# Kernel tuning notes

Measured on AMD Instinct MI355X. Metric: run time of the kernel, lower is better.

## Reference

```python
import jax, jax.numpy as jnp
import numpy as np

B, N, D = 1, 4096, 512
H, HD = 8, 64
NBINS = 512
CAND = 64
SCALE = 1.0 / np.sqrt(HD)
MAX_NORM = 1.0 - 1e-5
TWO_PI = 2.0 * np.pi


def _project(x):
    # Poincare-ball style projection: clip L2 norm of each point to MAX_NORM.
    n = jnp.sqrt(jnp.sum(x * x, axis=-1, keepdims=True))
    s = jnp.minimum(1.0, MAX_NORM / jnp.maximum(n, 1e-12))
    return x * s


def _bins(x):
    # Deterministic geometric binning (DavisCache stand-in): quantize the
    # angle of the first two coordinates into NBINS bins.
    ang = jnp.arctan2(x[..., 1], x[..., 0])  # (-pi, pi]
    b = jnp.floor((ang / TWO_PI + 0.5) * NBINS)
    return jnp.clip(b, 0, NBINS - 1).astype(jnp.int32)


def setup_inputs() -> dict:
    key0 = jax.random.key(0)
    ks = jax.random.split(key0, 12)
    w = 0.02  # typical init scale for projection weights
    return {
        "query": jax.random.normal(ks[0], (B, N, D), dtype=jnp.float32),
        "key": jax.random.normal(ks[1], (B, N, D), dtype=jnp.float32),
        "value": jax.random.normal(ks[2], (B, N, D), dtype=jnp.float32),
        "Wq": jax.random.normal(ks[3], (D, D), dtype=jnp.float32) * w,
        "bq": jnp.zeros((D,), dtype=jnp.float32),
        "Wk": jax.random.normal(ks[4], (D, D), dtype=jnp.float32) * w,
        "bk": jnp.zeros((D,), dtype=jnp.float32),
        "Wv": jax.random.normal(ks[5], (D, D), dtype=jnp.float32) * w,
        "bv": jnp.zeros((D,), dtype=jnp.float32),
        "Wo": jax.random.normal(ks[6], (D, D), dtype=jnp.float32) * w,
        "bo": jnp.zeros((D,), dtype=jnp.float32),
    }


def reference(query, key, value, Wq, bq, Wk, bk, Wv, bv, Wo, bo):
    Bq, Nq, Dm = query.shape
    Nk = key.shape[1]
    # projections + split heads -> (B, H, N, HD)
    q = (query @ Wq.T + bq).reshape(Bq, Nq, H, HD).transpose(0, 2, 1, 3)
    k = (key @ Wk.T + bk).reshape(Bq, Nk, H, HD).transpose(0, 2, 1, 3)
    v = (value @ Wv.T + bv).reshape(Bq, Nk, H, HD).transpose(0, 2, 1, 3)
    q = _project(q)
    k = _project(k)

    # geometric binning; candidate keys for a query are those whose bin is
    # within radius 1 of the query's bin (neighboring_bins, radius=1).
    qb = _bins(q)  # (B, H, Nq) int32
    kb = _bins(k)  # (B, H, Nk) int32
    mask = jnp.abs(qb[..., :, None] - kb[..., None, :]) <= 1  # (B,H,Nq,Nk)
    # fallback: if a query has no candidates, attend over all keys
    any_valid = jnp.any(mask, axis=-1, keepdims=True)
    eff = jnp.where(any_valid, mask, True)
    # keep only the first CAND candidates per query (by key index)
    rank = jnp.cumsum(eff.astype(jnp.int32), axis=-1) - 1
    sel = eff & (rank < CAND)

    scores = jnp.einsum("bhqd,bhkd->bhqk", q, k) * SCALE
    scores = jnp.where(sel, scores, -jnp.inf)
    attn = jax.nn.softmax(scores, axis=-1)  # dropout p=0.0 (eval mode)
    out = jnp.einsum("bhqk,bhkd->bhqd", attn, v)

    out = out.transpose(0, 2, 1, 3).reshape(Bq, Nq, Dm)
    return out @ Wo.T + bo
```

## Files before the change

### kernel.cpp

```cpp
#include <hip/hip_runtime.h>
#include <math.h>

typedef unsigned short u16;
typedef __attribute__((ext_vector_type(8))) short v8bf;
typedef __attribute__((ext_vector_type(4))) float f32x4;

#define N_TOK 4096
#define DMODEL 512
#define NHEAD 8
#define HDIM 64
#define CANDN 64
#define NBINS 512
#define BINCAP 64
#define QCAP 128
#define ATT_SCALE 0.125f
#define MAX_NORM_F 0.99999f

__device__ __forceinline__ float bf2f(u16 u) {
  union { unsigned int i; float f; } v; v.i = ((unsigned int)u) << 16; return v.f;
}
__device__ __forceinline__ u16 f2bf(float f) {
  union { float f; unsigned int i; } v; v.f = f;
  unsigned int x = v.i;
  return (u16)((x + 0x7fffu + ((x >> 16) & 1u)) >> 16);
}
__device__ __forceinline__ uint4 load_pack8(const float* __restrict__ p) {
  const float4 x0 = *(const float4*)p;
  const float4 x1 = *(const float4*)(p + 4);
  union { u16 h[8]; uint4 u; } r;
  r.h[0] = f2bf(x0.x); r.h[1] = f2bf(x0.y); r.h[2] = f2bf(x0.z); r.h[3] = f2bf(x0.w);
  r.h[4] = f2bf(x1.x); r.h[5] = f2bf(x1.y); r.h[6] = f2bf(x1.z); r.h[7] = f2bf(x1.w);
  return r.u;
}

__device__ __forceinline__ void gload16(const u16* __restrict__ g, u16* l) {
  __builtin_amdgcn_global_load_lds(
      (const __attribute__((address_space(1))) void*)g,
      (__attribute__((address_space(3))) void*)l, 16, 0, 0);
}

__global__ __launch_bounds__(256) void prep_kernel(
    const float* __restrict__ query, const float* __restrict__ key_,
    const float* __restrict__ value,
    const float* __restrict__ Wq, const float* __restrict__ Wk,
    const float* __restrict__ Wv, const float* __restrict__ Wo,
    u16* __restrict__ qx, u16* __restrict__ kx, u16* __restrict__ vx,
    u16* __restrict__ wqx, u16* __restrict__ wkx, u16* __restrict__ wvx,
    u16* __restrict__ wox,
    int* __restrict__ qb, int* __restrict__ kb, unsigned char* __restrict__ flags,
    int* __restrict__ khist)
{
  __shared__ float xs[16 * 516];
  const int blk = blockIdx.x;
  const int tid = threadIdx.x;

  if (blk >= 4096) {
    int4 z4; z4.x = 0; z4.y = 0; z4.z = 0; z4.w = 0;
    ((int4*)khist)[((blk - 4096) << 8) + tid] = z4;
    return;
  }

  if (blk >= 512) {
    const int rel = blk - 512;
    const float* src; u16* dst; int base;
    if (rel < 1024)      { src = query; dst = qx; base = rel << 11; }
    else if (rel < 2048) { src = key_;  dst = kx; base = (rel - 1024) << 11; }
    else if (rel < 3072) { src = value; dst = vx; base = (rel - 2048) << 11; }
    else {
      const int r2 = rel - 3072; const int w = r2 >> 7;
      src = (w == 0) ? Wq : (w == 1) ? Wk : (w == 2) ? Wv : Wo;
      dst = (w == 0) ? wqx : (w == 1) ? wkx : (w == 2) ? wvx : wox;
      base = (r2 & 127) << 11;
    }
    const int off = base + tid * 8;
    *(uint4*)(dst + off) = load_pack8(src + off);
    return;
  }

  const int isk  = blk >> 8;
  const int tile = blk & 255;
  const float* X = isk ? key_ : query;
  const float* W = isk ? Wk : Wq;

#pragma unroll
  for (int i = 0; i < 8; ++i) {
    const int flat = i * 1024 + tid * 4;
    const int row = flat >> 9, col = flat & 511;
    *(float4*)&xs[row * 516 + col] = *(const float4*)(X + (tile * 16 + row) * DMODEL + col);
  }
  __syncthreads();

  const int n_local = tid >> 4;
  const int pair = tid & 15;
  const int h = pair >> 1, coord = pair & 1;
  const float* wrow = W + ((h << 6) + coord) * DMODEL;
  const float* xrow = &xs[n_local * 516];

  double c0 = 0.0, c1 = 0.0, c2 = 0.0, c3 = 0.0;
  for (int k = 0; k < DMODEL; k += 4) {
    const float4 xv = *(const float4*)(xrow + k);
    const float4 wv = *(const float4*)(wrow + k);
    c0 = fma((double)xv.x, (double)wv.x, c0);
    c1 = fma((double)xv.y, (double)wv.y, c1);
    c2 = fma((double)xv.z, (double)wv.z, c2);
    c3 = fma((double)xv.w, (double)wv.w, c3);
  }
  const double a = (c0 + c1) + (c2 + c3);
  const double other = __shfl_xor(a, 1);
  if (coord == 0) {
    const double a0 = a, a1 = other;
    const int n = tile * 16 + n_local;
    double ang = atan2(a1, a0);
    double t = (ang / 6.283185307179586 + 0.5) * 512.0;
    int b = (int)floor(t);
    b = b < 0 ? 0 : (b > 511 ? 511 : b);
    (isk ? kb : qb)[(h << 12) + n] = b;

    const double r = sqrt(a0 * a0 + a1 * a1);
    const double dist = fabs(t - nearbyint(t));
    const double margin = fmin(0.45, 3.3e-4 / fmax(r, 1e-30) + 5e-5);
    flags[(isk << 15) | (h << 12) | n] = (dist < margin) ? 1 : 0;
  }
}

__device__ float fdlibm_atanf(float x) {
#pragma clang fp contract(off)
  const float atanhi[4] = {4.6364760399e-01f, 7.8539812565e-01f,
                           9.8279368877e-01f, 1.5707962513e+00f};
  const float atanlo[4] = {5.0121582440e-09f, 3.7748947079e-08f,
                           3.4473217170e-08f, 7.5497894159e-08f};
  const float aT[5] = {3.3333328366e-01f, -1.9999158382e-01f, 1.4253635705e-01f,
                       -1.0648017377e-01f, 6.1687607318e-02f};
  unsigned ix = __float_as_uint(x);
  const unsigned sign = ix >> 31;
  ix &= 0x7fffffffu;
  int id;
  float z, w, s1, s2;
  if (ix >= 0x4c800000u) {
    z = atanhi[3] + 0x1p-120f;
    return sign ? -z : z;
  }
  if (ix < 0x3ee00000u) {
    if (ix < 0x39800000u) return x;
    id = -1;
  } else {
    x = fabsf(x);
    if (ix < 0x3f980000u) {
      if (ix < 0x3f300000u) { id = 0; x = (2.0f * x - 1.0f) / (2.0f + x); }
      else                  { id = 1; x = (x - 1.0f) / (x + 1.0f); }
    } else {
      if (ix < 0x401c0000u) { id = 2; x = (x - 1.5f) / (1.0f + 1.5f * x); }
      else                  { id = 3; x = -1.0f / x; }
    }
  }
  z = x * x;
  w = z * z;
  s1 = z * (aT[0] + w * (aT[2] + w * aT[4]));
  s2 = w * (aT[1] + w * aT[3]);
  if (id < 0) return x - x * (s1 + s2);
  z = atanhi[id] - ((x * (s1 + s2) - atanlo[id]) - x);
  return sign ? -z : z;
}

__device__ float fdlibm_atan2f(float y, float x) {
#pragma clang fp contract(off)
  const float pi = 3.1415927410e+00f, pi_lo = -8.7422776573e-08f;
  const unsigned hx = __float_as_uint(x), hy = __float_as_uint(y);
  if (hx == 0x3f800000u) return fdlibm_atanf(y);
  const unsigned m = ((hy >> 31) & 1u) | ((hx >> 30) & 2u);
  const unsigned ix = hx & 0x7fffffffu, iy = hy & 0x7fffffffu;
  if (iy == 0u) {
    switch (m) { case 0: case 1: return y; case 2: return pi; default: return -pi; }
  }
  if (ix == 0u) return (m & 1u) ? -1.57079637050628662f : 1.57079637050628662f;
  float z;
  if (ix + (26u << 23) < iy) {
    z = 1.57079637050628662f;
    return (m & 1u) ? -z : z;
  }
  if ((m & 2u) && iy + (26u << 23) < ix) z = 0.0f;
  else z = fdlibm_atanf(fabsf(y / x));
  switch (m) {
    case 0: return z;
    case 1: return -z;
    case 2: return pi - (z - pi_lo);
    default: return (z - pi_lo) - pi;
  }
}

__global__ __launch_bounds__(256) void gemmfix_kernel(
    const u16* __restrict__ qx, const u16* __restrict__ kx, const u16* __restrict__ vx,
    const u16* __restrict__ wqx, const u16* __restrict__ wkx, const u16* __restrict__ wvx,
    const float* __restrict__ bq, const float* __restrict__ bk, const float* __restrict__ bv,
    const float* __restrict__ query, const float* __restrict__ key_,
    const float* __restrict__ Wq, const float* __restrict__ Wk,
    const unsigned char* __restrict__ flags,
    int* __restrict__ qb, int* __restrict__ kb,
    u16* __restrict__ Qb, u16* __restrict__ Kb, u16* __restrict__ Vb)
{
  __shared__ u16 As[128 * 32];
  __shared__ u16 Ws[128 * 32];
  __shared__ int wle[64];
  __shared__ int wlc;

  const int blk = blockIdx.x;
  const int tid = threadIdx.x;

  if (blk >= 384) {
    const int slice = blk - 384;
    if (tid == 0) wlc = 0;
    __syncthreads();
    for (int i = tid; i < 1024; i += 256) {
      const int flat = slice * 1024 + i;
      if (flags[flat]) {
        const int p = atomicAdd(&wlc, 1);
        if (p < 64) wle[p] = flat;
      }
    }
    __syncthreads();
    int nw = wlc; if (nw > 64) nw = 64;
    const int w = tid >> 6, d = tid & 63;
    for (int e = w; e < nw; e += 4) {
      const int flat = wle[e];
      const int n = flat & 4095;
      const int h = (flat >> 12) & 7;
      const int isk = flat >> 15;
      const float* xr = (isk ? key_ : query) + n * DMODEL;
      const float* wr = (isk ? Wk : Wq) + ((h << 6) + d) * DMODEL;
      float acc = 0.0f;
      for (int k = 0; k < DMODEL; k += 16) {
        const float4 xa = *(const float4*)(xr + k);
        const float4 xb = *(const float4*)(xr + k + 4);
        const float4 xc = *(const float4*)(xr + k + 8);
        const float4 xd = *(const float4*)(xr + k + 12);
        const float4 wa = *(const float4*)(wr + k);
        const float4 wb = *(const float4*)(wr + k + 4);
        const float4 wc = *(const float4*)(wr + k + 8);
        const float4 wd = *(const float4*)(wr + k + 12);
        acc = __fmaf_rn(xa.x, wa.x, acc); acc = __fmaf_rn(xa.y, wa.y, acc);
        acc = __fmaf_rn(xa.z, wa.z, acc); acc = __fmaf_rn(xa.w, wa.w, acc);
        acc = __fmaf_rn(xb.x, wb.x, acc); acc = __fmaf_rn(xb.y, wb.y, acc);
        acc = __fmaf_rn(xb.z, wb.z, acc); acc = __fmaf_rn(xb.w, wb.w, acc);
        acc = __fmaf_rn(xc.x, wc.x, acc); acc = __fmaf_rn(xc.y, wc.y, acc);
        acc = __fmaf_rn(xc.z, wc.z, acc); acc = __fmaf_rn(xc.w, wc.w, acc);
        acc = __fmaf_rn(xd.x, wd.x, acc); acc = __fmaf_rn(xd.y, wd.y, acc);
        acc = __fmaf_rn(xd.z, wd.z, acc); acc = __fmaf_rn(xd.w, wd.w, acc);
      }
      {
#pragma clang fp contract(off)
        const float sq = acc * acc;
        float rr[8];
#pragma unroll
        for (int j = 0; j < 8; ++j) rr[j] = __shfl(sq, j);
        for (int i = 8; i < 64; i += 8) {
#pragma unroll
          for (int j = 0; j < 8; ++j) rr[j] += __shfl(sq, i + j);
        }
        const float ss = ((rr[0] + rr[1]) + (rr[2] + rr[3])) +
                         ((rr[4] + rr[5]) + (rr[6] + rr[7]));
        const float nrm = __fsqrt_rn(ss);
        const float s = fminf(1.0f, 0.99999f / fmaxf(nrm, 1e-12f));
        const float c0 = __shfl(acc, 0) * s;
        const float c1 = __shfl(acc, 1) * s;
        const float cr = (float)atan2((double)c1, (double)c0);
        const float fd = fdlibm_atan2f(c1, c0);
        const float tol = fmaxf(fabsf(cr) * 6e-7f, 1e-30f);
        const float ang = (fabsf(fd - cr) <= tol) ? fd : cr;
        const float t = ((ang / 6.2831854820251465f) + 0.5f) * 512.0f;
        int b = (int)floorf(t);
        b = b < 0 ? 0 : (b > 511 ? 511 : b);
        if (d == 0) (isk ? kb : qb)[(h << 12) + n] = b;
      }
    }
    return;
  }

  const int z = blk >> 7;
  const int rem = blk & 127;
  const int bm = (rem & 31) * 128;
  const int bn = (rem >> 5) * 128;

  const u16* A    = (z == 0) ? qx : (z == 1) ? kx : vx;
  const u16* W    = (z == 0) ? wqx : (z == 1) ? wkx : wvx;
  const float* bias = (z == 0) ? bq : (z == 1) ? bk : bv;
  u16* O          = (z == 0) ? Qb : (z == 1) ? Kb : Vb;

  const int lane = tid & 63;
  const int wave = tid >> 6;
  const int wm = (wave & 1) * 64;
  const int wn = (wave >> 1) * 64;
  const int l15 = lane & 15;
  const int quad = lane >> 4;

  const int ca = tid;
  const int cb = tid + 256;
  const int ra = ca >> 2, oa = (ca & 3) * 8;
  const int rb = cb >> 2, ob = (cb & 3) * 8;

  f32x4 acc[4][4] = {};

  for (int kt = 0; kt < DMODEL; kt += 32) {
    __syncthreads();
    gload16(A + (bm + ra) * DMODEL + kt + oa, &As[ca * 8]);
    gload16(A + (bm + rb) * DMODEL + kt + ob, &As[cb * 8]);
    gload16(W + (bn + ra) * DMODEL + kt + oa, &Ws[ca * 8]);
    gload16(W + (bn + rb) * DMODEL + kt + ob, &Ws[cb * 8]);
    __syncthreads();
    v8bf af[4], bfr[4];
#pragma unroll
    for (int i = 0; i < 4; ++i)
      af[i] = *(const v8bf*)&As[(wm + i * 16 + l15) * 32 + quad * 8];
#pragma unroll
    for (int j = 0; j < 4; ++j)
      bfr[j] = *(const v8bf*)&Ws[(wn + j * 16 + l15) * 32 + quad * 8];
#pragma unroll
    for (int i = 0; i < 4; ++i)
#pragma unroll
      for (int j = 0; j < 4; ++j)
        acc[i][j] = __builtin_amdgcn_mfma_f32_16x16x32_bf16(af[i], bfr[j], acc[i][j], 0, 0, 0);
  }

  float bval[4];
#pragma unroll
  for (int j = 0; j < 4; ++j) bval[j] = bias[bn + wn + j * 16 + l15];
  const int h = (bn + wn) >> 6;

#pragma unroll
  for (int i = 0; i < 4; ++i) {
#pragma unroll
    for (int r = 0; r < 4; ++r) {
      const int row = bm + wm + i * 16 + quad * 4 + r;
      float v0 = acc[i][0][r] + bval[0];
      float v1 = acc[i][1][r] + bval[1];
      float v2 = acc[i][2][r] + bval[2];
      float v3 = acc[i][3][r] + bval[3];
      if (z != 2) {
        float ss = v0 * v0 + v1 * v1 + v2 * v2 + v3 * v3;
#pragma unroll
        for (int o = 1; o < 16; o <<= 1) ss += __shfl_xor(ss, o);
        const float s = fminf(1.0f, MAX_NORM_F / fmaxf(sqrtf(ss), 1e-12f));
        v0 *= s; v1 *= s; v2 *= s; v3 *= s;
      }
      const int base = (((h << 12) + row) << 6) + l15;
      O[base +  0] = f2bf(v0); O[base + 16] = f2bf(v1);
      O[base + 32] = f2bf(v2); O[base + 48] = f2bf(v3);
    }
  }
}

__global__ __launch_bounds__(256) void bin_hist_kernel(
    const int* __restrict__ kb, const int* __restrict__ qb,
    int* __restrict__ khist, u16* __restrict__ blist,
    int* __restrict__ qhist, u16* __restrict__ qlist)
{
  const int h = blockIdx.x;
  const int type = blockIdx.y;
  const int* src = type ? qb : kb;
  int* hist = type ? qhist : khist;
  u16* list = type ? qlist : blist;
  const int cap = type ? QCAP : BINCAP;

  const int i = blockIdx.z * 256 + threadIdx.x;
  const int b = src[(h << 12) + i];
  const int pos = atomicAdd(&hist[(h << 9) + b], 1);
  if (pos < cap) list[((h << 9) + b) * cap + pos] = (u16)i;
}

__global__ __launch_bounds__(64) void attn_bin_kernel(
    const u16* __restrict__ Qb, const u16* __restrict__ Kb,
    const u16* __restrict__ Vb, const int* __restrict__ qhist,
    const u16* __restrict__ qlist, const int* __restrict__ khist,
    const u16* __restrict__ blist, u16* __restrict__ aout)
{
  __shared__ u16 kf[4 * 2 * 4 * 16 * 8];
  __shared__ u16 vf[4 * 2 * 4 * 16 * 8];
  __shared__ u16 pf[16 * 72];
  __shared__ u16 s_cand[64];
  __shared__ int s_qg[16];

  const int hb = blockIdx.x;
  const int h = hb >> 9;
  const int b = hb & 511;
  int qcnt = qhist[hb];
  if (qcnt > QCAP) qcnt = QCAP;
  if (qcnt == 0) return;

  const int lane = threadIdx.x;
  const int l15 = lane & 15;
  const int quad = lane >> 4;

  int v0 = 0xFFFF, v1 = 0xFFFF, v2 = 0xFFFF;
  int c0 = 0, c1 = 0, c2 = 0;
  if (b > 0) {
    c0 = khist[(h << 9) + b - 1];
    if (c0 > BINCAP) c0 = BINCAP;
    if (lane < c0) v0 = (int)blist[(((h << 9) + b - 1) << 6) + lane];
  }
  {
    c1 = khist[(h << 9) + b];
    if (c1 > BINCAP) c1 = BINCAP;
    if (lane < c1) v1 = (int)blist[(((h << 9) + b) << 6) + lane];
  }
  if (b < NBINS - 1) {
    c2 = khist[(h << 9) + b + 1];
    if (c2 > BINCAP) c2 = BINCAP;
    if (lane < c2) v2 = (int)blist[(((h << 9) + b + 1) << 6) + lane];
  }

  int r0 = 0, r1 = 0, r2 = 0;
#pragma unroll 8
  for (int j = 0; j < 64; ++j) {
    const int w0 = __shfl(v0, j);
    const int w1 = __shfl(v1, j);
    const int w2 = __shfl(v2, j);
    r0 += (w0 < v0) + (w1 < v0) + (w2 < v0);
    r1 += (w0 < v1) + (w1 < v1) + (w2 < v1);
    r2 += (w0 < v2) + (w1 < v2) + (w2 < v2);
  }
  const int tot = c0 + c1 + c2;
  const int ccnt = tot < CANDN ? tot : CANDN;
  const int ccnt_eff = (tot == 0) ? 64 : ccnt;
  if (tot == 0) {
    s_cand[lane] = (u16)lane;
  } else {
    if (v0 != 0xFFFF && r0 < CANDN) s_cand[r0] = (u16)v0;
    if (v1 != 0xFFFF && r1 < CANDN) s_cand[r1] = (u16)v1;
    if (v2 != 0xFFFF && r2 < CANDN) s_cand[r2] = (u16)v2;
  }
  __syncthreads();
  if (tot > 0 && lane >= ccnt) s_cand[lane] = s_cand[0];
  __syncthreads();

  {
    const int r = lane >> 3, s = lane & 7;
    const int ks = s >> 2, qd = s & 3;
#pragma unroll
    for (int it = 0; it < 8; ++it) {
      const int key = it * 8 + r;
      const int c = s_cand[key];
      const uint4 kv = *(const uint4*)(Kb + ((h << 18) | (c << 6)) + s * 8);
      const int idx = ((((key >> 4) * 2 + ks) * 4 + qd) * 16 + (key & 15)) * 8;
      *(uint4*)&kf[idx] = kv;
    }
  }
  {
    const int r = lane >> 3, s = lane & 7;
    const int nt = s >> 1, d0 = (s & 1) * 8;
#pragma unroll
    for (int it = 0; it < 8; ++it) {
      const int key = it * 8 + r;
      const int c = s_cand[key];
      union { u16 hh[8]; uint4 u; } vv;
      vv.u = *(const uint4*)(Vb + ((h << 18) | (c << 6)) + s * 8);
      const int kstep = key >> 5, qd = (key >> 3) & 3, j = key & 7;
#pragma unroll
      for (int m = 0; m < 8; ++m)
        vf[(((nt * 2 + kstep) * 4 + qd) * 16 + d0 + m) * 8 + j] = vv.hh[m];
    }
  }
  __syncthreads();

  v8bf akf[4][2], bvf[4][2];
#pragma unroll
  for (int t = 0; t < 4; ++t)
#pragma unroll
    for (int ks = 0; ks < 2; ++ks) {
      akf[t][ks] = *(const v8bf*)&kf[(((t * 2 + ks) * 4 + quad) * 16 + l15) * 8];
      bvf[t][ks] = *(const v8bf*)&vf[(((t * 2 + ks) * 4 + quad) * 16 + l15) * 8];
    }

  const int nchunk = (qcnt + 15) >> 4;
  for (int ci = 0; ci < nchunk; ++ci) {
    const int base = ci << 4;
    const int qcn = min(16, qcnt - base);
    __syncthreads();
    if (lane < 16) {
      int idx = base + lane;
      if (idx > qcnt - 1) idx = qcnt - 1;
      s_qg[lane] = (int)qlist[(hb << 7) + idx];
    }
    __syncthreads();

    const u16* qrow = Qb + ((h << 18) | (s_qg[l15] << 6));
    v8bf bq[2];
#pragma unroll
    for (int ks = 0; ks < 2; ++ks)
      bq[ks] = *(const v8bf*)(qrow + ks * 32 + quad * 8);

    float sc[16];
#pragma unroll
    for (int t = 0; t < 4; ++t) {
      f32x4 sa = {0.f, 0.f, 0.f, 0.f};
      sa = __builtin_amdgcn_mfma_f32_16x16x32_bf16(akf[t][0], bq[0], sa, 0, 0, 0);
      sa = __builtin_amdgcn_mfma_f32_16x16x32_bf16(akf[t][1], bq[1], sa, 0, 0, 0);
#pragma unroll
      for (int r = 0; r < 4; ++r) {
        const int key = t * 16 + quad * 4 + r;
        sc[t * 4 + r] = (key < ccnt_eff) ? sa[r] * ATT_SCALE : -INFINITY;
      }
    }
    float mx = sc[0];
#pragma unroll
    for (int i = 1; i < 16; ++i) mx = fmaxf(mx, sc[i]);
    mx = fmaxf(mx, __shfl_xor(mx, 16));
    mx = fmaxf(mx, __shfl_xor(mx, 32));
    float sum = 0.0f;
    float pe[16];
#pragma unroll
    for (int i = 0; i < 16; ++i) { pe[i] = __expf(sc[i] - mx); sum += pe[i]; }
    sum += __shfl_xor(sum, 16);
    sum += __shfl_xor(sum, 32);
    const float inv = 1.0f / sum;

    __syncthreads();
#pragma unroll
    for (int t = 0; t < 4; ++t)
#pragma unroll
      for (int r = 0; r < 4; ++r)
        pf[l15 * 72 + t * 16 + quad * 4 + r] = f2bf(pe[t * 4 + r] * inv);
    __syncthreads();

    v8bf ap[2];
#pragma unroll
    for (int ks = 0; ks < 2; ++ks)
      ap[ks] = *(const v8bf*)&pf[l15 * 72 + ks * 32 + quad * 8];

#pragma unroll
    for (int nt = 0; nt < 4; ++nt) {
      f32x4 o = {0.f, 0.f, 0.f, 0.f};
      o = __builtin_amdgcn_mfma_f32_16x16x32_bf16(ap[0], bvf[nt][0], o, 0, 0, 0);
      o = __builtin_amdgcn_mfma_f32_16x16x32_bf16(ap[1], bvf[nt][1], o, 0, 0, 0);
#pragma unroll
      for (int r = 0; r < 4; ++r) {
        const int row = quad * 4 + r;
        if (row < qcn)
          aout[s_qg[row] * DMODEL + (h << 6) + nt * 16 + l15] = f2bf(o[r]);
      }
    }
  }
}

__global__ __launch_bounds__(256) void gemm_out_kernel(
    const u16* __restrict__ A, const u16* __restrict__ W,
    const float* __restrict__ bias, float* __restrict__ O)
{
  __shared__ u16 As[128 * 32];
  __shared__ u16 Ws[128 * 32];

  const int tid  = threadIdx.x;
  const int lane = tid & 63;
  const int wave = tid >> 6;

  const int bm = blockIdx.x * 128;
  const int bn = blockIdx.y * 128;
  const int wm = (wave & 1) * 64;
  const int wn = (wave >> 1) * 64;
  const int l15 = lane & 15;
  const int quad = lane >> 4;

  const int ca = tid;
  const int cb = tid + 256;
  const int ra = ca >> 2, oa = (ca & 3) * 8;
  const int rb = cb >> 2, ob = (cb & 3) * 8;

  f32x4 acc[4][4] = {};

  for (int kt = 0; kt < DMODEL; kt += 32) {
    __syncthreads();
    gload16(A + (bm + ra) * DMODEL + kt + oa, &As[ca * 8]);
    gload16(A + (bm + rb) * DMODEL + kt + ob, &As[cb * 8]);
    gload16(W + (bn + ra) * DMODEL + kt + oa, &Ws[ca * 8]);
    gload16(W + (bn + rb) * DMODEL + kt + ob, &Ws[cb * 8]);
    __syncthreads();
    v8bf af[4], bfr[4];
#pragma unroll
    for (int i = 0; i < 4; ++i)
      af[i] = *(const v8bf*)&As[(wm + i * 16 + l15) * 32 + quad * 8];
#pragma unroll
    for (int j = 0; j < 4; ++j)
      bfr[j] = *(const v8bf*)&Ws[(wn + j * 16 + l15) * 32 + quad * 8];
#pragma unroll
    for (int i = 0; i < 4; ++i)
#pragma unroll
      for (int j = 0; j < 4; ++j)
        acc[i][j] = __builtin_amdgcn_mfma_f32_16x16x32_bf16(af[i], bfr[j], acc[i][j], 0, 0, 0);
  }

#pragma unroll
  for (int j = 0; j < 4; ++j) {
    const int cg = bn + wn + j * 16 + l15;
    const float bval = bias[cg];
#pragma unroll
    for (int i = 0; i < 4; ++i) {
      const int rbase = bm + wm + i * 16 + quad * 4;
#pragma unroll
      for (int r = 0; r < 4; ++r)
        O[(rbase + r) * DMODEL + cg] = acc[i][j][r] + bval;
    }
  }
}

extern "C" void kernel_launch(void* const* d_in, const int* in_sizes, int n_in,
                              void* d_out, int out_size, void* d_ws, size_t ws_size,
                              hipStream_t stream) {
  const float* query = (const float*)d_in[0];
  const float* key_  = (const float*)d_in[1];
  const float* value = (const float*)d_in[2];
  const float* Wq = (const float*)d_in[3];
  const float* bq = (const float*)d_in[4];
  const float* Wk = (const float*)d_in[5];
  const float* bk = (const float*)d_in[6];
  const float* Wv = (const float*)d_in[7];
  const float* bv = (const float*)d_in[8];
  const float* Wo = (const float*)d_in[9];
  const float* bo = (const float*)d_in[10];

  char* ws = (char*)d_ws;
  u16* qx    = (u16*)(ws);
  u16* kx    = (u16*)(ws + 4194304);
  u16* vx    = (u16*)(ws + 8388608);
  u16* wqx   = (u16*)(ws + 12582912);
  u16* wkx   = (u16*)(ws + 13107200);
  u16* wvx   = (u16*)(ws + 13631488);
  u16* wox   = (u16*)(ws + 14155776);
  u16* Qb    = (u16*)(ws + 14680064);
  u16* Kb    = (u16*)(ws + 18874368);
  u16* Vb    = (u16*)(ws + 23068672);
  u16* aout  = (u16*)(ws + 27262976);
  int* qb    = (int*)(ws + 31457280);
  int* kb    = (int*)(ws + 31588352);
  unsigned char* flags = (unsigned char*)(ws + 31719424);
  int* khist = (int*)(ws + 31784960);
  int* qhist = (int*)(ws + 31801344);
  u16* blist = (u16*)(ws + 31817728);
  u16* qlist = (u16*)(ws + 32342016);

  prep_kernel<<<4104, 256, 0, stream>>>(
      query, key_, value, Wq, Wk, Wv, Wo,
      qx, kx, vx, wqx, wkx, wvx, wox, qb, kb, flags, khist);
  gemmfix_kernel<<<448, 256, 0, stream>>>(
      qx, kx, vx, wqx, wkx, wvx, bq, bk, bv,
      query, key_, Wq, Wk, flags, qb, kb, Qb, Kb, Vb);
  bin_hist_kernel<<<dim3(8, 2, 16), 256, 0, stream>>>(
      kb, qb, khist, blist, qhist, qlist);
  attn_bin_kernel<<<4096, 64, 0, stream>>>(
      Qb, Kb, Vb, qhist, qlist, khist, blist, aout);
  gemm_out_kernel<<<dim3(32, 4), 256, 0, stream>>>(aout, wox, bo, (float*)d_out);
}
```

Before: 212.6 us.

## Double-buffer GEMM tiles via register prefetch with padded LDS, add MFMA priority

Both bf16 GEMM kernels (QKV projection and output projection) stop using direct global-to-LDS loads with two barriers per k-step. They now prefetch the next k-tile into registers while the current tile is consumed from a ping-pong LDS buffer, which leaves one barrier per step. Row stride is padded from 32 to 40 elements to reduce LDS bank conflicts on the fragment reads. The attention kernel also raises wave priority around its MFMA sections. This costs more LDS and registers per block, which could lower occupancy.

```diff
diff --git a/kernel.cpp b/kernel.cpp
--- a/kernel.cpp
+++ b/kernel.cpp
@@ -31,12 +31,6 @@
   r.h[0] = f2bf(x0.x); r.h[1] = f2bf(x0.y); r.h[2] = f2bf(x0.z); r.h[3] = f2bf(x0.w);
   r.h[4] = f2bf(x1.x); r.h[5] = f2bf(x1.y); r.h[6] = f2bf(x1.z); r.h[7] = f2bf(x1.w);
   return r.u;
-}
-
-__device__ __forceinline__ void gload16(const u16* __restrict__ g, u16* l) {
-  __builtin_amdgcn_global_load_lds(
-      (const __attribute__((address_space(1))) void*)g,
-      (__attribute__((address_space(3))) void*)l, 16, 0, 0);
 }
 
 __global__ __launch_bounds__(256) void prep_kernel(
@@ -198,8 +192,8 @@
     int* __restrict__ qb, int* __restrict__ kb,
     u16* __restrict__ Qb, u16* __restrict__ Kb, u16* __restrict__ Vb)
 {
-  __shared__ u16 As[128 * 32];
-  __shared__ u16 Ws[128 * 32];
+  __shared__ u16 As[2][128 * 40];
+  __shared__ u16 Ws[2][128 * 40];
   __shared__ int wle[64];
   __shared__ int wlc;
 
@@ -287,32 +281,40 @@
 
   const int lane = tid & 63;
   const int wave = tid >> 6;
+  const int row4 = tid >> 2;
+  const int seg  = tid & 3;
   const int wm = (wave & 1) * 64;
   const int wn = (wave >> 1) * 64;
   const int l15 = lane & 15;
   const int quad = lane >> 4;
 
-  const int ca = tid;
-  const int cb = tid + 256;
-  const int ra = ca >> 2, oa = (ca & 3) * 8;
-  const int rb = cb >> 2, ob = (cb & 3) * 8;
-
   f32x4 acc[4][4] = {};
 
+  uint4 a0 = *(const uint4*)(A + (bm + row4) * DMODEL + seg * 8);
+  uint4 a1 = *(const uint4*)(A + (bm + row4 + 64) * DMODEL + seg * 8);
+  uint4 w0 = *(const uint4*)(W + (bn + row4) * DMODEL + seg * 8);
+  uint4 w1 = *(const uint4*)(W + (bn + row4 + 64) * DMODEL + seg * 8);
+
   for (int kt = 0; kt < DMODEL; kt += 32) {
-    __syncthreads();
-    gload16(A + (bm + ra) * DMODEL + kt + oa, &As[ca * 8]);
-    gload16(A + (bm + rb) * DMODEL + kt + ob, &As[cb * 8]);
-    gload16(W + (bn + ra) * DMODEL + kt + oa, &Ws[ca * 8]);
-    gload16(W + (bn + rb) * DMODEL + kt + ob, &Ws[cb * 8]);
-    __syncthreads();
+    const int p = (kt >> 5) & 1;
+    *(uint4*)&As[p][row4 * 40 + seg * 8] = a0;
+    *(uint4*)&As[p][(row4 + 64) * 40 + seg * 8] = a1;
+    *(uint4*)&Ws[p][row4 * 40 + seg * 8] = w0;
+    *(uint4*)&Ws[p][(row4 + 64) * 40 + seg * 8] = w1;
+    __syncthreads();
+    if (kt + 32 < DMODEL) {
+      a0 = *(const uint4*)(A + (bm + row4) * DMODEL + kt + 32 + seg * 8);
+      a1 = *(const uint4*)(A + (bm + row4 + 64) * DMODEL + kt + 32 + seg * 8);
+      w0 = *(const uint4*)(W + (bn + row4) * DMODEL + kt + 32 + seg * 8);
+      w1 = *(const uint4*)(W + (bn + row4 + 64) * DMODEL + kt + 32 + seg * 8);
+    }
     v8bf af[4], bfr[4];
 #pragma unroll
     for (int i = 0; i < 4; ++i)
-      af[i] = *(const v8bf*)&As[(wm + i * 16 + l15) * 32 + quad * 8];
+      af[i] = *(const v8bf*)&As[p][(wm + i * 16 + l15) * 40 + quad * 8];
 #pragma unroll
     for (int j = 0; j < 4; ++j)
-      bfr[j] = *(const v8bf*)&Ws[(wn + j * 16 + l15) * 32 + quad * 8];
+      bfr[j] = *(const v8bf*)&Ws[p][(wn + j * 16 + l15) * 40 + quad * 8];
 #pragma unroll
     for (int i = 0; i < 4; ++i)
 #pragma unroll
@@ -488,6 +490,7 @@
       bq[ks] = *(const v8bf*)(qrow + ks * 32 + quad * 8);
 
     float sc[16];
+    __builtin_amdgcn_s_setprio(1);
 #pragma unroll
     for (int t = 0; t < 4; ++t) {
       f32x4 sa = {0.f, 0.f, 0.f, 0.f};
@@ -499,6 +502,7 @@
         sc[t * 4 + r] = (key < ccnt_eff) ? sa[r] * ATT_SCALE : -INFINITY;
       }
     }
+    __builtin_amdgcn_s_setprio(0);
     float mx = sc[0];
 #pragma unroll
     for (int i = 1; i < 16; ++i) mx = fmaxf(mx, sc[i]);
@@ -525,6 +529,7 @@
     for (int ks = 0; ks < 2; ++ks)
       ap[ks] = *(const v8bf*)&pf[l15 * 72 + ks * 32 + quad * 8];
 
+    __builtin_amdgcn_s_setprio(1);
 #pragma unroll
     for (int nt = 0; nt < 4; ++nt) {
       f32x4 o = {0.f, 0.f, 0.f, 0.f};
@@ -537,6 +542,7 @@
           aout[s_qg[row] * DMODEL + (h << 6) + nt * 16 + l15] = f2bf(o[r]);
       }
     }
+    __builtin_amdgcn_s_setprio(0);
   }
 }
 
@@ -544,12 +550,14 @@
     const u16* __restrict__ A, const u16* __restrict__ W,
     const float* __restrict__ bias, float* __restrict__ O)
 {
-  __shared__ u16 As[128 * 32];
-  __shared__ u16 Ws[128 * 32];
+  __shared__ u16 As[2][128 * 40];
+  __shared__ u16 Ws[2][128 * 40];
 
   const int tid  = threadIdx.x;
   const int lane = tid & 63;
   const int wave = tid >> 6;
+  const int row4 = tid >> 2;
+  const int seg  = tid & 3;
 
   const int bm = blockIdx.x * 128;
   const int bn = blockIdx.y * 128;
@@ -558,27 +566,33 @@
   const int l15 = lane & 15;
   const int quad = lane >> 4;
 
-  const int ca = tid;
-  const int cb = tid + 256;
-  const int ra = ca >> 2, oa = (ca & 3) * 8;
-  const int rb = cb >> 2, ob = (cb & 3) * 8;
-
   f32x4 acc[4][4] = {};
 
+  uint4 a0 = *(const uint4*)(A + (bm + row4) * DMODEL + seg * 8);
+  uint4 a1 = *(const uint4*)(A + (bm + row4 + 64) * DMODEL + seg * 8);
+  uint4 w0 = *(const uint4*)(W + (bn + row4) * DMODEL + seg * 8);
+  uint4 w1 = *(const uint4*)(W + (bn + row4 + 64) * DMODEL + seg * 8);
+
   for (int kt = 0; kt < DMODEL; kt += 32) {
-    __syncthreads();
-    gload16(A + (bm + ra) * DMODEL + kt + oa, &As[ca * 8]);
-    gload16(A + (bm + rb) * DMODEL + kt + ob, &As[cb * 8]);
-    gload16(W + (bn + ra) * DMODEL + kt + oa, &Ws[ca * 8]);
-    gload16(W + (bn + rb) * DMODEL + kt + ob, &Ws[cb * 8]);
-    __syncthreads();
+    const int p = (kt >> 5) & 1;
+    *(uint4*)&As[p][row4 * 40 + seg * 8] = a0;
+    *(uint4*)&As[p][(row4 + 64) * 40 + seg * 8] = a1;
+    *(uint4*)&Ws[p][row4 * 40 + seg * 8] = w0;
+    *(uint4*)&Ws[p][(row4 + 64) * 40 + seg * 8] = w1;
+    __syncthreads();
+    if (kt + 32 < DMODEL) {
+      a0 = *(const uint4*)(A + (bm + row4) * DMODEL + kt + 32 + seg * 8);
+      a1 = *(const uint4*)(A + (bm + row4 + 64) * DMODEL + kt + 32 + seg * 8);
+      w0 = *(const uint4*)(W + (bn + row4) * DMODEL + kt + 32 + seg * 8);
+      w1 = *(const uint4*)(W + (bn + row4 + 64) * DMODEL + kt + 32 + seg * 8);
+    }
     v8bf af[4], bfr[4];
 #pragma unroll
     for (int i = 0; i < 4; ++i)
-      af[i] = *(const v8bf*)&As[(wm + i * 16 + l15) * 32 + quad * 8];
+      af[i] = *(const v8bf*)&As[p][(wm + i * 16 + l15) * 40 + quad * 8];
 #pragma unroll
     for (int j = 0; j < 4; ++j)
-      bfr[j] = *(const v8bf*)&Ws[(wn + j * 16 + l15) * 32 + quad * 8];
+      bfr[j] = *(const v8bf*)&Ws[p][(wn + j * 16 + l15) * 40 + quad * 8];
 #pragma unroll
     for (int i = 0; i < 4; ++i)
 #pragma unroll
```

After: 213.1 us. About the same (+0.2%).
